# Optimization experiments

Hardware: AMD Instinct MI355X
Metric: run time of the kernel (lower is better)

## Reference

```python
import jax, jax.numpy as jnp
import numpy as np

B, N, E, H, SD, HID = 4, 512, 1024, 16, 64, 64
D = E // H  # head_dim


def setup_inputs() -> dict:
    key = jax.random.key(0)
    ks = jax.random.split(key, 20)
    s = lambda i, shape, scale: (jax.random.normal(ks[i], shape, dtype=jnp.float32) * scale)
    inp = {
        "query": s(0, (B, N, E), 1.0),
        "key": s(1, (B, N, E), 1.0),
        "value": s(2, (B, N, E), 1.0),
        "state_embeddings": s(3, (B, N, SD), 1.0),
        # projection weights stored [in, out] (transposed vs torch nn.Linear)
        "Wq": s(4, (E, E), E ** -0.5), "bq": jnp.zeros((E,), jnp.float32),
        "Wk": s(5, (E, E), E ** -0.5), "bk": jnp.zeros((E,), jnp.float32),
        "Wv": s(6, (E, E), E ** -0.5), "bv": jnp.zeros((E,), jnp.float32),
        "Wo": s(7, (E, E), E ** -0.5), "bo": jnp.zeros((E,), jnp.float32),
        # CAB compatibility MLP: Linear(2*SD->HID), ReLU, Linear(HID->HID), ReLU, Linear(HID->H)
        "W1": s(8, (2 * SD, HID), (2 * SD) ** -0.5), "b1": jnp.zeros((HID,), jnp.float32),
        "W2": s(9, (HID, HID), HID ** -0.5), "b2": jnp.zeros((HID,), jnp.float32),
        "W3": s(10, (HID, H), HID ** -0.5), "b3": jnp.zeros((H,), jnp.float32),
        "head_temps": jnp.ones((H,), jnp.float32),
    }
    return inp


def reference(query, key, value, state_embeddings,
              Wq, bq, Wk, bk, Wv, bv, Wo, bo,
              W1, b1, W2, b2, W3, b3, head_temps):
    scale = D ** -0.5
    q = (query @ Wq + bq).reshape(B, N, H, D)
    k = (key @ Wk + bk).reshape(B, N, H, D)
    v = (value @ Wv + bv).reshape(B, N, H, D)
    # [B, H, T, S]
    scores = jnp.einsum("bthd,bshd->bhts", q, k) * scale

    # CAB bias: MLP([e_i; e_j]) -> split first layer to avoid materializing pairs
    hi = state_embeddings @ W1[:SD]          # [B, N, HID]
    hj = state_embeddings @ W1[SD:]          # [B, N, HID]
    h = jax.nn.relu(hi[:, :, None, :] + hj[:, None, :, :] + b1)  # [B, N, N, HID]
    h = jax.nn.relu(h @ W2 + b2)
    comp = h @ W3 + b3                        # [B, N, N, H]
    bias = jnp.transpose(comp, (0, 3, 1, 2)) * head_temps[None, :, None, None]
    scores = scores + bias

    attn = jax.nn.softmax(scores, axis=-1)
    out = jnp.einsum("bhts,bshd->bthd", attn, v).reshape(B, N, E)
    return out @ Wo + bo
```

## Files before the change

kernel.cpp:

```cpp
#include <hip/hip_runtime.h>
#include <hip/hip_bf16.h>

typedef unsigned short u16;
typedef short short8 __attribute__((ext_vector_type(8)));
typedef float f32x4 __attribute__((ext_vector_type(4)));
typedef unsigned short u16x4 __attribute__((ext_vector_type(4)));

#define BB 4
#define NS 512
#define EE 1024
#define HH 16
#define DD 64
#define MM (BB*NS)
#define NSQ 2
#define SQW (NS/NSQ)

__device__ __forceinline__ u16 f2bfh(float x) {
  __hip_bfloat16 h = __float2bfloat16(x);
  union { __hip_bfloat16 h; u16 u; } c; c.h = h; return c.u;
}
__device__ __forceinline__ unsigned pkbf(float a, float b) {
  union { __hip_bfloat16 h; u16 u; } ca, cb;
  ca.h = __float2bfloat16(a); cb.h = __float2bfloat16(b);
  return (unsigned)ca.u | ((unsigned)cb.u << 16);
}
union S8 { short8 s; unsigned u[4]; };

__device__ __forceinline__ void gload_lds16(const void* g, void* l) {
  __builtin_amdgcn_global_load_lds(
      (const __attribute__((address_space(1))) unsigned int*)g,
      (__attribute__((address_space(3))) unsigned int*)l, 16, 0, 0);
}


__global__ void cvt_w(const float* __restrict__ Wq, const float* __restrict__ Wk,
                      const float* __restrict__ Wv, const float* __restrict__ Wo,
                      const float* __restrict__ W2, const float* __restrict__ W3,
                      const float* __restrict__ q, const float* __restrict__ k,
                      const float* __restrict__ v,
                      u16* __restrict__ WqT, u16* __restrict__ WkT,
                      u16* __restrict__ WvT, u16* __restrict__ WoT,
                      u16* __restrict__ W2T, u16* __restrict__ W3P,
                      u16* __restrict__ qb, u16* __restrict__ kb, u16* __restrict__ vb) {
  int z = blockIdx.z;
  if (z >= 5) {
    int seg = z - 5;
    const float* src = seg == 0 ? q : (seg == 1 ? k : v);
    u16* dst = seg == 0 ? qb : (seg == 1 ? kb : vb);
    size_t flat = ((size_t)blockIdx.y * 32 + blockIdx.x) * 256 + threadIdx.x;
    size_t off = flat << 3;
    float4 f0 = *(const float4*)(src + off);
    float4 f1 = *(const float4*)(src + off + 4);
    S8 r;
    r.u[0] = pkbf(f0.x, f0.y); r.u[1] = pkbf(f0.z, f0.w);
    r.u[2] = pkbf(f1.x, f1.y); r.u[3] = pkbf(f1.z, f1.w);
    *(short8*)(dst + off) = r.s;
    return;
  }
  if (z == 4) {
    if (blockIdx.x || blockIdx.y) return;
    int tid = threadIdx.x;
    for (int i = tid; i < 4096; i += 256) {
      int n = i >> 6, kk = i & 63;
      W2T[i] = f2bfh(W2[kk * 64 + n]);
    }
    for (int i = tid; i < 1024; i += 256) {
      int h = i >> 6, rem = i & 63;
      int k2 = rem >> 5, gg = (rem >> 3) & 3, j = rem & 7;
      int c = (2 * k2 + (j >> 2)) * 16 + gg * 4 + (j & 3);
      W3P[i] = f2bfh(W3[c * 16 + h]);
    }
    return;
  }
  const float* W = z == 0 ? Wq : z == 1 ? Wk : z == 2 ? Wv : Wo;
  u16* WT = z == 0 ? WqT : z == 1 ? WkT : z == 2 ? WvT : WoT;
  int n0 = blockIdx.x << 5, k0 = blockIdx.y << 5;
  __shared__ float tile[32][33];
  int tx = threadIdx.x & 31, ty = threadIdx.x >> 5;
  #pragma unroll
  for (int i = 0; i < 4; ++i) {
    int r = (i << 3) + ty;
    tile[r][tx] = W[(size_t)(k0 + r) * EE + n0 + tx];
  }
  __syncthreads();
  #pragma unroll
  for (int i = 0; i < 4; ++i) {
    int r = (i << 3) + ty;
    WT[(size_t)(n0 + r) * EE + k0 + tx] = f2bfh(tile[tx][r]);
  }
}


__global__ void hi_hj_kernel(const float* __restrict__ se, const float* __restrict__ W1,
                             const float* __restrict__ b1,
                             float* __restrict__ hi, float* __restrict__ hj) {
  int tid = threadIdx.x;
  int row = blockIdx.x * 4 + (tid >> 6);
  int c = tid & 63;
  float ah = b1[c], aj = 0.f;
  #pragma unroll 8
  for (int k = 0; k < 64; ++k) {
    float s = se[row * 64 + k];
    ah += s * W1[k * 64 + c];
    aj += s * W1[(k + 64) * 64 + c];
  }
  hi[row * 64 + c] = ah;
  hj[row * 64 + c] = aj;
}


template <int MODE>
__device__ __forceinline__ void gemm_body(const u16* __restrict__ A, const u16* __restrict__ Bt,
                                          const float* __restrict__ bias, void* __restrict__ Cout) {
  __shared__ u16 As[128 * 32];
  __shared__ u16 Bs[128 * 32];
  const int tid = threadIdx.x, lane = tid & 63, wave = tid >> 6;
  const int m0 = blockIdx.x * 128, n0 = blockIdx.y * 128;
  const int wr = wave >> 1, wc = wave & 1;

  const f32x4 zero = {0.f, 0.f, 0.f, 0.f};
  f32x4 acc[4][4];
  #pragma unroll
  for (int i = 0; i < 4; ++i)
    #pragma unroll
    for (int j = 0; j < 4; ++j) acc[i][j] = zero;

  const int rA = lane >> 2;
  const int cA = (lane & 3) << 3;

  for (int kt = 0; kt < EE; kt += 32) {
    #pragma unroll
    for (int i = 0; i < 2; ++i) {
      int base = ((i << 2) + wave) << 9;
      int row = (base >> 5) + rA;
      gload_lds16(A  + (size_t)(m0 + row) * EE + kt + cA, As + base);
      gload_lds16(Bt + (size_t)(n0 + row) * EE + kt + cA, Bs + base);
    }
    __syncthreads();
    short8 af[4], bfr[4];
    #pragma unroll
    for (int mf = 0; mf < 4; ++mf) {
      int row = wr * 64 + mf * 16 + (lane & 15);
      af[mf] = *(const short8*)(As + row * 32 + ((lane >> 4) << 3));
    }
    #pragma unroll
    for (int nf = 0; nf < 4; ++nf) {
      int row = wc * 64 + nf * 16 + (lane & 15);
      bfr[nf] = *(const short8*)(Bs + row * 32 + ((lane >> 4) << 3));
    }
    #pragma unroll
    for (int mf = 0; mf < 4; ++mf)
      #pragma unroll
      for (int nf = 0; nf < 4; ++nf)
        acc[mf][nf] = __builtin_amdgcn_mfma_f32_16x16x32_bf16(af[mf], bfr[nf], acc[mf][nf], 0, 0, 0);
    __syncthreads();
  }

  #pragma unroll
  for (int mf = 0; mf < 4; ++mf) {
    #pragma unroll
    for (int nf = 0; nf < 4; ++nf) {
      int col = n0 + wc * 64 + nf * 16 + (lane & 15);
      float bv = bias[col];
      #pragma unroll
      for (int j = 0; j < 4; ++j) {
        int rowm = m0 + wr * 64 + mf * 16 + ((lane >> 4) << 2) + j;
        float v = acc[mf][nf][j] + bv;
        int bb = rowm >> 9, r = rowm & 511;
        int h = col >> 6, d = col & 63;
        size_t off;
        if (MODE == 0)
          off = ((((size_t)bb * HH + h) * 32 + (r >> 4)) << 10) + ((size_t)(d >> 5) << 9)
              + ((size_t)((((d >> 3) & 3) << 4) + (r & 15)) << 3) + (d & 7);
        else
          off = (((((size_t)bb * HH + h) * 16 + (r >> 5)) * 4 + (d >> 4)) << 9)
              + ((size_t)((((r >> 3) & 3) << 4) + (d & 15)) << 3) + (r & 7);
        ((u16*)Cout)[off] = f2bfh(v);
      }
    }
  }
}

__global__ __launch_bounds__(256, 2) void gemm_proj(
    const u16* __restrict__ qb, const u16* __restrict__ kb, const u16* __restrict__ vb,
    const u16* __restrict__ WqT, const u16* __restrict__ WkT, const u16* __restrict__ WvT,
    const float* __restrict__ bq, const float* __restrict__ bk, const float* __restrict__ bv_,
    u16* __restrict__ qF, u16* __restrict__ kF, u16* __restrict__ vF) {
  int z = blockIdx.z;
  if (z == 0)      gemm_body<0>(qb, WqT, bq, qF);
  else if (z == 1) gemm_body<0>(kb, WkT, bk, kF);
  else             gemm_body<1>(vb, WvT, bv_, vF);
}


__global__ __launch_bounds__(256, 2) void gemm_final64(
    const u16* __restrict__ A, const u16* __restrict__ Bt,
    const float* __restrict__ bias, float* __restrict__ C) {
  __shared__ u16 As[64 * 32];
  __shared__ u16 Bs[128 * 32];
  const int tid = threadIdx.x, lane = tid & 63, wave = tid >> 6;
  const int m0 = blockIdx.x * 64, n0 = blockIdx.y * 128;
  const int wr = wave >> 1, wc = wave & 1;

  const f32x4 zero = {0.f, 0.f, 0.f, 0.f};
  f32x4 acc[2][4];
  #pragma unroll
  for (int i = 0; i < 2; ++i)
    #pragma unroll
    for (int j = 0; j < 4; ++j) acc[i][j] = zero;

  const int rA = lane >> 2;
  const int cA = (lane & 3) << 3;

  for (int kt = 0; kt < EE; kt += 32) {
    {
      int base = wave << 9;
      int row = (wave << 4) + rA;
      gload_lds16(A + (size_t)(m0 + row) * EE + kt + cA, As + base);
    }
    #pragma unroll
    for (int i = 0; i < 2; ++i) {
      int base = ((i << 2) + wave) << 9;
      int row = (base >> 5) + rA;
      gload_lds16(Bt + (size_t)(n0 + row) * EE + kt + cA, Bs + base);
    }
    __syncthreads();
    short8 af[2], bfr[4];
    #pragma unroll
    for (int mf = 0; mf < 2; ++mf) {
      int row = wr * 32 + mf * 16 + (lane & 15);
      af[mf] = *(const short8*)(As + row * 32 + ((lane >> 4) << 3));
    }
    #pragma unroll
    for (int nf = 0; nf < 4; ++nf) {
      int row = wc * 64 + nf * 16 + (lane & 15);
      bfr[nf] = *(const short8*)(Bs + row * 32 + ((lane >> 4) << 3));
    }
    #pragma unroll
    for (int mf = 0; mf < 2; ++mf)
      #pragma unroll
      for (int nf = 0; nf < 4; ++nf)
        acc[mf][nf] = __builtin_amdgcn_mfma_f32_16x16x32_bf16(af[mf], bfr[nf], acc[mf][nf], 0, 0, 0);
    __syncthreads();
  }

  #pragma unroll
  for (int mf = 0; mf < 2; ++mf)
    #pragma unroll
    for (int nf = 0; nf < 4; ++nf) {
      int col = n0 + wc * 64 + nf * 16 + (lane & 15);
      float bv = bias[col];
      #pragma unroll
      for (int j = 0; j < 4; ++j) {
        int rowm = m0 + wr * 32 + mf * 16 + ((lane >> 4) << 2) + j;
        C[(size_t)rowm * EE + col] = acc[mf][nf][j] + bv;
      }
    }
}


__global__ __launch_bounds__(512, 2) void fused_cab_attn(
    const float* __restrict__ hi, const float* __restrict__ hj,
    const u16* __restrict__ W2T, const u16* __restrict__ W3P,
    const float* __restrict__ b2, const float* __restrict__ b3,
    const float* __restrict__ temps,
    const u16* __restrict__ qF, const u16* __restrict__ kF,
    const u16* __restrict__ vF,
    float* __restrict__ Opart, float* __restrict__ mlpart) {
  const int b = blockIdx.x >> 1, sq = blockIdx.x & 1, tt = blockIdx.y;
  const int t0 = tt << 4;
  const int tid = threadIdx.x, lane = tid & 63, wave = tid >> 6;
  const int g = lane >> 4, sl = lane & 15;

  __shared__ float hi_s[16][80];
  __shared__ float hj_s[2][32][65];
  __shared__ float b2_s[64], b3_s[16], tp_s[16];
  __shared__ float comp3[16 * 273];
  __shared__ u16 Pl[8][16][40];

  if (tid < 256) {
    int r = tid >> 4, c4 = (tid & 15) << 2;
    float4 hv = *(const float4*)(hi + ((size_t)(b * NS + t0 + r) << 6) + c4);
    *(f32x4*)&hi_s[r][c4] = (f32x4){hv.x, hv.y, hv.z, hv.w};
  } else {
    int ix = tid - 256;
    if (ix < 64) b2_s[ix] = b2[ix];
    else if (ix < 80) b3_s[ix - 64] = b3[ix - 64];
    else if (ix < 96) tp_s[ix - 80] = temps[ix - 80];
  }

  const int hr = tid >> 4, hc4 = (tid & 15) << 2;
  {
    float4 a = *(const float4*)(hj + ((size_t)(b * NS + sq * SQW + hr) << 6) + hc4);
    hj_s[0][hr][hc4 + 0] = a.x; hj_s[0][hr][hc4 + 1] = a.y;
    hj_s[0][hr][hc4 + 2] = a.z; hj_s[0][hr][hc4 + 3] = a.w;
  }

  const f32x4 zero = {0.f, 0.f, 0.f, 0.f};
  f32x4 acc[2][4];
  #pragma unroll
  for (int i = 0; i < 2; ++i)
    #pragma unroll
    for (int j = 0; j < 4; ++j) acc[i][j] = zero;
  float m_run[2] = {-3e38f, -3e38f};
  float l_run[2] = {0.f, 0.f};

  int cur = 0;
  for (int pr = 0; pr < 8; ++pr) {
    const int s0p = sq * SQW + (pr << 5);
    __syncthreads();

    float4 hjnx;
    const bool have = (pr + 1) < 8;
    if (have)
      hjnx = *(const float4*)(hj + ((size_t)(b * NS + s0p + 32 + hr) << 6) + hc4);

    float vsc[2][2][4];

    #pragma unroll
    for (int ta = 0; ta < 2; ++ta) {
      if (ta) __syncthreads();
      {
        float hjv[2][8];
        #pragma unroll
        for (int kk = 0; kk < 2; ++kk)
          #pragma unroll
          for (int j = 0; j < 8; ++j)
            hjv[kk][j] = hj_s[cur][(ta << 4) + sl][kk * 32 + (g << 3) + j];

        short8 w3f[2];
        #pragma unroll
        for (int k2 = 0; k2 < 2; ++k2)
          w3f[k2] = *(const short8*)(W3P + (sl << 6) + k2 * 32 + (g << 3));

        float b2v[4][4];
        #pragma unroll
        for (int mfc = 0; mfc < 4; ++mfc)
          #pragma unroll
          for (int jj = 0; jj < 4; ++jj)
            b2v[mfc][jj] = b2_s[mfc * 16 + (g << 2) + jj];

        #pragma unroll
        for (int q = 0; q < 2; ++q) {
          int tl = (wave << 1) + q;
          short8 xb[2];
          #pragma unroll
          for (int kk = 0; kk < 2; ++kk) {
            int c0 = kk * 32 + (g << 3);
            f32x4 h0 = *(const f32x4*)&hi_s[tl][c0];
            f32x4 h1 = *(const f32x4*)&hi_s[tl][c0 + 4];
            float x[8];
            #pragma unroll
            for (int j = 0; j < 4; ++j) {
              x[j]     = fmaxf(h0[j] + hjv[kk][j], 0.f);
              x[j + 4] = fmaxf(h1[j] + hjv[kk][j + 4], 0.f);
            }
            S8 r;
            r.u[0] = pkbf(x[0], x[1]); r.u[1] = pkbf(x[2], x[3]);
            r.u[2] = pkbf(x[4], x[5]); r.u[3] = pkbf(x[6], x[7]);
            xb[kk] = r.s;
          }
          f32x4 accY[4];
          #pragma unroll
          for (int i = 0; i < 4; ++i) accY[i] = zero;
          #pragma unroll
          for (int kk = 0; kk < 2; ++kk)
            #pragma unroll
            for (int mfc = 0; mfc < 4; ++mfc) {
              short8 w2 = *(const short8*)(W2T + ((mfc * 16 + sl) << 6) + kk * 32 + (g << 3));
              accY[mfc] = __builtin_amdgcn_mfma_f32_16x16x32_bf16(w2, xb[kk], accY[mfc], 0, 0, 0);
            }
          f32x4 compD = zero;
          #pragma unroll
          for (int k2 = 0; k2 < 2; ++k2) {
            float y[8];
            #pragma unroll
            for (int j = 0; j < 4; ++j) {
              y[j]     = fmaxf(accY[2 * k2][j]     + b2v[2 * k2][j],     0.f);
              y[j + 4] = fmaxf(accY[2 * k2 + 1][j] + b2v[2 * k2 + 1][j], 0.f);
            }
            S8 r;
            r.u[0] = pkbf(y[0], y[1]); r.u[1] = pkbf(y[2], y[3]);
            r.u[2] = pkbf(y[4], y[5]); r.u[3] = pkbf(y[6], y[7]);
            compD = __builtin_amdgcn_mfma_f32_16x16x32_bf16(w3f[k2], r.s, compD, 0, 0, 0);
          }
          #pragma unroll
          for (int jj = 0; jj < 4; ++jj) {
            int h = (g << 2) + jj;
            comp3[h * 273 + sl * 17 + tl] = (compD[jj] + b3_s[h]) * tp_s[h];
          }
        }
      }
      __syncthreads();
      const int s16 = (sq << 4) + (pr << 1) + ta;
      #pragma unroll
      for (int hh = 0; hh < 2; ++hh) {
        int h = (wave << 1) + hh;
        const u16* qb_ = qF + ((((size_t)b * HH + h) * 32 + tt) << 10) + (lane << 3);
        const u16* kb_ = kF + ((((size_t)b * HH + h) * 32 + s16) << 10) + (lane << 3);
        f32x4 accS = zero;
        accS = __builtin_amdgcn_mfma_f32_16x16x32_bf16(*(const short8*)kb_, *(const short8*)qb_, accS, 0, 0, 0);
        accS = __builtin_amdgcn_mfma_f32_16x16x32_bf16(*(const short8*)(kb_ + 512), *(const short8*)(qb_ + 512), accS, 0, 0, 0);
        #pragma unroll
        for (int j = 0; j < 4; ++j)
          vsc[ta][hh][j] = accS[j] * 0.125f + comp3[h * 273 + ((g << 2) + j) * 17 + sl];
      }
    }

    if (have) {
      hj_s[cur ^ 1][hr][hc4 + 0] = hjnx.x; hj_s[cur ^ 1][hr][hc4 + 1] = hjnx.y;
      hj_s[cur ^ 1][hr][hc4 + 2] = hjnx.z; hj_s[cur ^ 1][hr][hc4 + 3] = hjnx.w;
    }

    #pragma unroll
    for (int hh = 0; hh < 2; ++hh) {
      int h = (wave << 1) + hh;
      float e[8];
      float mx = -3e38f;
      #pragma unroll
      for (int j = 0; j < 4; ++j)
        mx = fmaxf(mx, fmaxf(vsc[0][hh][j], vsc[1][hh][j]));
      mx = fmaxf(mx, __shfl_xor(mx, 16, 64));
      mx = fmaxf(mx, __shfl_xor(mx, 32, 64));
      float mnew = fmaxf(m_run[hh], mx);
      float c = __expf(m_run[hh] - mnew);
      m_run[hh] = mnew;
      #pragma unroll
      for (int ta = 0; ta < 2; ++ta)
        #pragma unroll
        for (int j = 0; j < 4; ++j)
          e[ta * 4 + j] = __expf(vsc[ta][hh][j] - mnew);
      float ps = ((e[0] + e[1]) + (e[2] + e[3])) + ((e[4] + e[5]) + (e[6] + e[7]));
      ps += __shfl_xor(ps, 16, 64);
      ps += __shfl_xor(ps, 32, 64);
      l_run[hh] = l_run[hh] * c + ps;

      uint2 wA; wA.x = pkbf(e[0], e[1]); wA.y = pkbf(e[2], e[3]);
      uint2 wB; wB.x = pkbf(e[4], e[5]); wB.y = pkbf(e[6], e[7]);
      *(uint2*)&Pl[wave][sl][(g << 2)]      = wA;
      *(uint2*)&Pl[wave][sl][16 + (g << 2)] = wB;
      short8 pf = *(const short8*)&Pl[wave][sl][(g << 3)];

      float cb[4];
      #pragma unroll
      for (int j = 0; j < 4; ++j) cb[j] = __shfl(c, (g << 2) + j, 64);

      const u16* vb0 = vF + (((((size_t)b * HH + h) * 16 + (sq << 3) + pr) * 4) << 9) + (lane << 3);
      #pragma unroll
      for (int nf = 0; nf < 4; ++nf) {
        #pragma unroll
        for (int j = 0; j < 4; ++j) acc[hh][nf][j] *= cb[j];
        short8 vv = *(const short8*)(vb0 + ((size_t)nf << 9));
        acc[hh][nf] = __builtin_amdgcn_mfma_f32_16x16x32_bf16(pf, vv, acc[hh][nf], 0, 0, 0);
      }
    }
    cur ^= 1;
  }

  size_t obase = ((size_t)sq * MM + (size_t)b * NS + t0) * EE;
  #pragma unroll
  for (int hh = 0; hh < 2; ++hh) {
    int h = (wave << 1) + hh;
    #pragma unroll
    for (int nf = 0; nf < 4; ++nf)
      #pragma unroll
      for (int j = 0; j < 4; ++j)
        Opart[obase + (size_t)((g << 2) + j) * EE + (h << 6) + nf * 16 + sl] = acc[hh][nf][j];
  }
  if (g == 0) {
    #pragma unroll
    for (int hh = 0; hh < 2; ++hh) {
      int h = (wave << 1) + hh;
      size_t mlb = (((size_t)sq * MM + b * NS + t0 + sl) * HH + h) * 2;
      mlpart[mlb] = m_run[hh];
      mlpart[mlb + 1] = l_run[hh];
    }
  }
}


__global__ void combine_pv(const float* __restrict__ Opart, const float* __restrict__ mlpart,
                           u16* __restrict__ attn_out) {
  int row = blockIdx.x;
  int tid = threadIdx.x;
  int c4 = tid << 2;
  int h = c4 >> 6;
  float m[NSQ], l[NSQ];
  #pragma unroll
  for (int pq = 0; pq < NSQ; ++pq) {
    size_t mb = (((size_t)pq * MM + row) * HH + h) * 2;
    m[pq] = mlpart[mb]; l[pq] = mlpart[mb + 1];
  }
  float M = m[0];
  #pragma unroll
  for (int pq = 1; pq < NSQ; ++pq) M = fmaxf(M, m[pq]);
  float den = 0.f;
  f32x4 num = {0.f, 0.f, 0.f, 0.f};
  #pragma unroll
  for (int pq = 0; pq < NSQ; ++pq) {
    float w = __expf(m[pq] - M);
    den += w * l[pq];
    f32x4 o = *(const f32x4*)(Opart + ((size_t)pq * MM + row) * EE + c4);
    #pragma unroll
    for (int i = 0; i < 4; ++i) num[i] += w * o[i];
  }
  float r = 1.0f / den;
  u16x4 out;
  #pragma unroll
  for (int i = 0; i < 4; ++i) out[i] = f2bfh(num[i] * r);
  *(u16x4*)(attn_out + (size_t)row * EE + c4) = out;
}


extern "C" void kernel_launch(void* const* d_in, const int* in_sizes, int n_in,
                              void* d_out, int out_size, void* d_ws, size_t ws_size,
                              hipStream_t stream) {
  const float* query = (const float*)d_in[0];
  const float* key   = (const float*)d_in[1];
  const float* value = (const float*)d_in[2];
  const float* se    = (const float*)d_in[3];
  const float* Wq = (const float*)d_in[4];  const float* bq = (const float*)d_in[5];
  const float* Wk = (const float*)d_in[6];  const float* bk = (const float*)d_in[7];
  const float* Wv = (const float*)d_in[8];  const float* bv = (const float*)d_in[9];
  const float* Wo = (const float*)d_in[10]; const float* bo = (const float*)d_in[11];
  const float* W1 = (const float*)d_in[12]; const float* b1 = (const float*)d_in[13];
  const float* W2 = (const float*)d_in[14]; const float* b2 = (const float*)d_in[15];
  const float* W3 = (const float*)d_in[16]; const float* b3 = (const float*)d_in[17];
  const float* temps = (const float*)d_in[18];

  char* p = (char*)d_ws;
  auto alloc = [&](size_t bytes) { char* r = p; p += (bytes + 255) & ~(size_t)255; return r; };
  u16* qb  = (u16*)alloc((size_t)MM * EE * 2);
  u16* kb  = (u16*)alloc((size_t)MM * EE * 2);
  u16* vb  = (u16*)alloc((size_t)MM * EE * 2);
  u16* WqT = (u16*)alloc((size_t)EE * EE * 2);
  u16* WkT = (u16*)alloc((size_t)EE * EE * 2);
  u16* WvT = (u16*)alloc((size_t)EE * EE * 2);
  u16* WoT = (u16*)alloc((size_t)EE * EE * 2);
  u16* W2T = (u16*)alloc(4096 * 2);
  u16* W3P = (u16*)alloc(1024 * 2);
  u16* qF  = (u16*)alloc((size_t)MM * EE * 2);
  u16* kF  = (u16*)alloc((size_t)MM * EE * 2);
  u16* vF  = (u16*)alloc((size_t)MM * EE * 2);
  float* hi = (float*)alloc((size_t)MM * 64 * 4);
  float* hj = (float*)alloc((size_t)MM * 64 * 4);
  float* Opart = (float*)alloc((size_t)NSQ * MM * EE * 4);
  float* mlpart = (float*)alloc((size_t)NSQ * MM * HH * 2 * 4);
  u16* attn_out = (u16*)alloc((size_t)MM * EE * 2);
  (void)ws_size; (void)in_sizes; (void)n_in; (void)out_size;

  cvt_w<<<dim3(32, 32, 8), 256, 0, stream>>>(Wq, Wk, Wv, Wo, W2, W3, query, key, value,
                                             WqT, WkT, WvT, WoT, W2T, W3P, qb, kb, vb);
  hi_hj_kernel<<<512, 256, 0, stream>>>(se, W1, b1, hi, hj);
  gemm_proj<<<dim3(16, 8, 3), 256, 0, stream>>>(qb, kb, vb, WqT, WkT, WvT, bq, bk, bv, qF, kF, vF);
  fused_cab_attn<<<dim3(8, 32, 1), 512, 0, stream>>>(hi, hj, W2T, W3P, b2, b3, temps,
                                                     qF, kF, vF, Opart, mlpart);
  combine_pv<<<MM, 256, 0, stream>>>(Opart, mlpart, attn_out);
  gemm_final64<<<dim3(32, 8), 256, 0, stream>>>(attn_out, WoT, bo, (float*)d_out);
}
```

Baseline: 114.9 us.

## Fuse split-softmax combine into output GEMM, fold hi/hj into convert, shrink proj tiles

```diff
diff --git a/kernel.cpp b/kernel.cpp
--- a/kernel.cpp
+++ b/kernel.cpp
@@ -38,11 +38,31 @@
                       const float* __restrict__ W2, const float* __restrict__ W3,
                       const float* __restrict__ q, const float* __restrict__ k,
                       const float* __restrict__ v,
+                      const float* __restrict__ se, const float* __restrict__ W1,
+                      const float* __restrict__ b1,
                       u16* __restrict__ WqT, u16* __restrict__ WkT,
                       u16* __restrict__ WvT, u16* __restrict__ WoT,
                       u16* __restrict__ W2T, u16* __restrict__ W3P,
-                      u16* __restrict__ qb, u16* __restrict__ kb, u16* __restrict__ vb) {
+                      u16* __restrict__ qb, u16* __restrict__ kb, u16* __restrict__ vb,
+                      float* __restrict__ hi, float* __restrict__ hj) {
   int z = blockIdx.z;
+  if (z == 8) {
+    int flat = blockIdx.y * 32 + blockIdx.x;
+    if (flat >= 512) return;
+    int tid = threadIdx.x;
+    int row = flat * 4 + (tid >> 6);
+    int c = tid & 63;
+    float ah = b1[c], aj = 0.f;
+    #pragma unroll 8
+    for (int kk = 0; kk < 64; ++kk) {
+      float s = se[row * 64 + kk];
+      ah += s * W1[kk * 64 + c];
+      aj += s * W1[(kk + 64) * 64 + c];
+    }
+    hi[row * 64 + c] = ah;
+    hj[row * 64 + c] = aj;
+    return;
+  }
   if (z >= 5) {
     int seg = z - 5;
     const float* src = seg == 0 ? q : (seg == 1 ? k : v);
@@ -91,37 +111,19 @@
 }
 
 
-__global__ void hi_hj_kernel(const float* __restrict__ se, const float* __restrict__ W1,
-                             const float* __restrict__ b1,
-                             float* __restrict__ hi, float* __restrict__ hj) {
-  int tid = threadIdx.x;
-  int row = blockIdx.x * 4 + (tid >> 6);
-  int c = tid & 63;
-  float ah = b1[c], aj = 0.f;
-  #pragma unroll 8
-  for (int k = 0; k < 64; ++k) {
-    float s = se[row * 64 + k];
-    ah += s * W1[k * 64 + c];
-    aj += s * W1[(k + 64) * 64 + c];
-  }
-  hi[row * 64 + c] = ah;
-  hj[row * 64 + c] = aj;
-}
-
-
 template <int MODE>
-__device__ __forceinline__ void gemm_body(const u16* __restrict__ A, const u16* __restrict__ Bt,
-                                          const float* __restrict__ bias, void* __restrict__ Cout) {
-  __shared__ u16 As[128 * 32];
+__device__ __forceinline__ void gemm_body64(const u16* __restrict__ A, const u16* __restrict__ Bt,
+                                            const float* __restrict__ bias, void* __restrict__ Cout) {
+  __shared__ u16 As[64 * 32];
   __shared__ u16 Bs[128 * 32];
   const int tid = threadIdx.x, lane = tid & 63, wave = tid >> 6;
-  const int m0 = blockIdx.x * 128, n0 = blockIdx.y * 128;
+  const int m0 = blockIdx.x * 64, n0 = blockIdx.y * 128;
   const int wr = wave >> 1, wc = wave & 1;
 
   const f32x4 zero = {0.f, 0.f, 0.f, 0.f};
-  f32x4 acc[4][4];
-  #pragma unroll
-  for (int i = 0; i < 4; ++i)
+  f32x4 acc[2][4];
+  #pragma unroll
+  for (int i = 0; i < 2; ++i)
     #pragma unroll
     for (int j = 0; j < 4; ++j) acc[i][j] = zero;
 
@@ -129,18 +131,22 @@
   const int cA = (lane & 3) << 3;
 
   for (int kt = 0; kt < EE; kt += 32) {
+    {
+      int base = wave << 9;
+      int row = (wave << 4) + rA;
+      gload_lds16(A + (size_t)(m0 + row) * EE + kt + cA, As + base);
+    }
     #pragma unroll
     for (int i = 0; i < 2; ++i) {
       int base = ((i << 2) + wave) << 9;
       int row = (base >> 5) + rA;
-      gload_lds16(A  + (size_t)(m0 + row) * EE + kt + cA, As + base);
       gload_lds16(Bt + (size_t)(n0 + row) * EE + kt + cA, Bs + base);
     }
     __syncthreads();
-    short8 af[4], bfr[4];
-    #pragma unroll
-    for (int mf = 0; mf < 4; ++mf) {
-      int row = wr * 64 + mf * 16 + (lane & 15);
+    short8 af[2], bfr[4];
+    #pragma unroll
+    for (int mf = 0; mf < 2; ++mf) {
+      int row = wr * 32 + mf * 16 + (lane & 15);
       af[mf] = *(const short8*)(As + row * 32 + ((lane >> 4) << 3));
     }
     #pragma unroll
@@ -149,7 +155,7 @@
       bfr[nf] = *(const short8*)(Bs + row * 32 + ((lane >> 4) << 3));
     }
     #pragma unroll
-    for (int mf = 0; mf < 4; ++mf)
+    for (int mf = 0; mf < 2; ++mf)
       #pragma unroll
       for (int nf = 0; nf < 4; ++nf)
         acc[mf][nf] = __builtin_amdgcn_mfma_f32_16x16x32_bf16(af[mf], bfr[nf], acc[mf][nf], 0, 0, 0);
@@ -157,14 +163,14 @@
   }
 
   #pragma unroll
-  for (int mf = 0; mf < 4; ++mf) {
+  for (int mf = 0; mf < 2; ++mf) {
     #pragma unroll
     for (int nf = 0; nf < 4; ++nf) {
       int col = n0 + wc * 64 + nf * 16 + (lane & 15);
       float bv = bias[col];
       #pragma unroll
       for (int j = 0; j < 4; ++j) {
-        int rowm = m0 + wr * 64 + mf * 16 + ((lane >> 4) << 2) + j;
+        int rowm = m0 + wr * 32 + mf * 16 + ((lane >> 4) << 2) + j;
         float v = acc[mf][nf][j] + bv;
         int bb = rowm >> 9, r = rowm & 511;
         int h = col >> 6, d = col & 63;
@@ -187,15 +193,16 @@
     const float* __restrict__ bq, const float* __restrict__ bk, const float* __restrict__ bv_,
     u16* __restrict__ qF, u16* __restrict__ kF, u16* __restrict__ vF) {
   int z = blockIdx.z;
-  if (z == 0)      gemm_body<0>(qb, WqT, bq, qF);
-  else if (z == 1) gemm_body<0>(kb, WkT, bk, kF);
-  else             gemm_body<1>(vb, WvT, bv_, vF);
-}
-
-
-__global__ __launch_bounds__(256, 2) void gemm_final64(
-    const u16* __restrict__ A, const u16* __restrict__ Bt,
-    const float* __restrict__ bias, float* __restrict__ C) {
+  if (z == 0)      gemm_body64<0>(qb, WqT, bq, qF);
+  else if (z == 1) gemm_body64<0>(kb, WkT, bk, kF);
+  else             gemm_body64<1>(vb, WvT, bv_, vF);
+}
+
+
+__global__ __launch_bounds__(256, 2) void gemm_final_comb(
+    const float* __restrict__ Opart, const float* __restrict__ mlpart,
+    const u16* __restrict__ Bt, const float* __restrict__ bias,
+    float* __restrict__ C) {
   __shared__ u16 As[64 * 32];
   __shared__ u16 Bs[128 * 32];
   const int tid = threadIdx.x, lane = tid & 63, wave = tid >> 6;
@@ -211,12 +218,36 @@
 
   const int rA = lane >> 2;
   const int cA = (lane & 3) << 3;
+  const int arow = m0 + (wave << 4) + rA;
+  const float* mlb = mlpart + (size_t)arow * (HH * 2);
+  const float* mlb1 = mlpart + ((size_t)MM + arow) * (HH * 2);
+  const float* O0r = Opart + (size_t)arow * EE;
+  const float* O1r = Opart + ((size_t)MM + arow) * EE;
+  u16* asdst = (u16*)As + (wave << 9) + (rA << 5) + cA;
 
   for (int kt = 0; kt < EE; kt += 32) {
     {
-      int base = wave << 9;
-      int row = (wave << 4) + rA;
-      gload_lds16(A + (size_t)(m0 + row) * EE + kt + cA, As + base);
+      int h = kt >> 6;
+      float ma = mlb[h * 2], la = mlb[h * 2 + 1];
+      float mbv = mlb1[h * 2], lb = mlb1[h * 2 + 1];
+      float M = fmaxf(ma, mbv);
+      float w0 = __expf(ma - M), w1 = __expf(mbv - M);
+      float r = 1.0f / (w0 * la + w1 * lb);
+      float a0 = w0 * r, a1 = w1 * r;
+      f32x4 x0 = *(const f32x4*)(O0r + kt + cA);
+      f32x4 x1 = *(const f32x4*)(O0r + kt + cA + 4);
+      f32x4 y0 = *(const f32x4*)(O1r + kt + cA);
+      f32x4 y1 = *(const f32x4*)(O1r + kt + cA + 4);
+      float e[8];
+      #pragma unroll
+      for (int j = 0; j < 4; ++j) {
+        e[j]     = a0 * x0[j] + a1 * y0[j];
+        e[j + 4] = a0 * x1[j] + a1 * y1[j];
+      }
+      S8 rr;
+      rr.u[0] = pkbf(e[0], e[1]); rr.u[1] = pkbf(e[2], e[3]);
+      rr.u[2] = pkbf(e[4], e[5]); rr.u[3] = pkbf(e[6], e[7]);
+      *(short8*)asdst = rr.s;
     }
     #pragma unroll
     for (int i = 0; i < 2; ++i) {
@@ -476,39 +507,6 @@
       mlpart[mlb + 1] = l_run[hh];
     }
   }
-}
-
-
-__global__ void combine_pv(const float* __restrict__ Opart, const float* __restrict__ mlpart,
-                           u16* __restrict__ attn_out) {
-  int row = blockIdx.x;
-  int tid = threadIdx.x;
-  int c4 = tid << 2;
-  int h = c4 >> 6;
-  float m[NSQ], l[NSQ];
-  #pragma unroll
-  for (int pq = 0; pq < NSQ; ++pq) {
-    size_t mb = (((size_t)pq * MM + row) * HH + h) * 2;
-    m[pq] = mlpart[mb]; l[pq] = mlpart[mb + 1];
-  }
-  float M = m[0];
-  #pragma unroll
-  for (int pq = 1; pq < NSQ; ++pq) M = fmaxf(M, m[pq]);
-  float den = 0.f;
-  f32x4 num = {0.f, 0.f, 0.f, 0.f};
-  #pragma unroll
-  for (int pq = 0; pq < NSQ; ++pq) {
-    float w = __expf(m[pq] - M);
-    den += w * l[pq];
-    f32x4 o = *(const f32x4*)(Opart + ((size_t)pq * MM + row) * EE + c4);
-    #pragma unroll
-    for (int i = 0; i < 4; ++i) num[i] += w * o[i];
-  }
-  float r = 1.0f / den;
-  u16x4 out;
-  #pragma unroll
-  for (int i = 0; i < 4; ++i) out[i] = f2bfh(num[i] * r);
-  *(u16x4*)(attn_out + (size_t)row * EE + c4) = out;
 }
 
 
@@ -546,15 +544,14 @@
   float* hj = (float*)alloc((size_t)MM * 64 * 4);
   float* Opart = (float*)alloc((size_t)NSQ * MM * EE * 4);
   float* mlpart = (float*)alloc((size_t)NSQ * MM * HH * 2 * 4);
-  u16* attn_out = (u16*)alloc((size_t)MM * EE * 2);
   (void)ws_size; (void)in_sizes; (void)n_in; (void)out_size;
 
-  cvt_w<<<dim3(32, 32, 8), 256, 0, stream>>>(Wq, Wk, Wv, Wo, W2, W3, query, key, value,
-                                             WqT, WkT, WvT, WoT, W2T, W3P, qb, kb, vb);
-  hi_hj_kernel<<<512, 256, 0, stream>>>(se, W1, b1, hi, hj);
-  gemm_proj<<<dim3(16, 8, 3), 256, 0, stream>>>(qb, kb, vb, WqT, WkT, WvT, bq, bk, bv, qF, kF, vF);
+  cvt_w<<<dim3(32, 32, 9), 256, 0, stream>>>(Wq, Wk, Wv, Wo, W2, W3, query, key, value,
+                                             se, W1, b1,
+                                             WqT, WkT, WvT, WoT, W2T, W3P, qb, kb, vb,
+                                             hi, hj);
+  gemm_proj<<<dim3(32, 8, 3), 256, 0, stream>>>(qb, kb, vb, WqT, WkT, WvT, bq, bk, bv, qF, kF, vF);
   fused_cab_attn<<<dim3(8, 32, 1), 512, 0, stream>>>(hi, hj, W2T, W3P, b2, b3, temps,
                                                      qF, kF, vF, Opart, mlpart);
-  combine_pv<<<MM, 256, 0, stream>>>(Opart, mlpart, attn_out);
-  gemm_final64<<<dim3(32, 8), 256, 0, stream>>>(attn_out, WoT, bo, (float*)d_out);
-}
+  gemm_final_comb<<<dim3(32, 8), 256, 0, stream>>>(Opart, mlpart, WoT, bo, (float*)d_out);
+}
```

Result: slower. 136.1 us (+18.4%).
